# Optimization experiments

Measured on AMD Instinct MI355X. Metric: run time of the kernel, lower is better.

Reference implementation:

```python
import jax, jax.numpy as jnp
import numpy as np

# module hyperparams (match init_kwargs)
C_IN = 256
HEADS = 8
HEAD_DIM = 32
PW, PH = 4, 4
TOPK = 2
SIM_POW = 2.0
SIDE = 64
T = SIDE * SIDE
B = 16


def setup_inputs() -> dict:
    key = jax.random.key(0)
    ks = jax.random.split(key, 7)
    hd = HEADS * HEAD_DIM
    s = 1.0 / np.sqrt(C_IN)
    return {
        "x": jax.random.normal(ks[0], (T, B, C_IN), dtype=jnp.float32),
        "f_w": jax.random.uniform(ks[1], (hd, C_IN), jnp.float32, -s, s),
        "f_b": jax.random.uniform(ks[2], (hd,), jnp.float32, -s, s),
        "v_w": jax.random.uniform(ks[3], (hd, C_IN), jnp.float32, -s, s),
        "v_b": jax.random.uniform(ks[4], (hd,), jnp.float32, -s, s),
        "proj_w": jax.random.uniform(ks[5], (C_IN, hd), jnp.float32, -1.0 / np.sqrt(hd), 1.0 / np.sqrt(hd)),
        "proj_b": jax.random.uniform(ks[6], (C_IN,), jnp.float32, -1.0 / np.sqrt(hd), 1.0 / np.sqrt(hd)),
        "sim_alpha": jnp.ones((1,), jnp.float32),
        "sim_beta": jnp.zeros((1,), jnp.float32),
    }


def _l2norm(z):
    # F.normalize with eps=1e-12
    n = jnp.linalg.norm(z, axis=-1, keepdims=True)
    return z / jnp.maximum(n, 1e-12)


def reference(x, f_w, f_b, v_w, v_b, proj_w, proj_b, sim_alpha, sim_beta):
    t, b, c = x.shape
    side = SIDE
    H, D = HEADS, HEAD_DIM
    M = PW * PH

    xt = jnp.transpose(x, (1, 0, 2))  # [B, T, C]
    q = xt @ f_w.T + f_b              # [B, T, H*D] (1x1 conv)
    v = xt @ v_w.T + v_b

    def split_heads(z):
        # [B,T,H*D] -> [B*H, side, side, D]
        z = z.reshape(b, side, side, H, D)
        return jnp.transpose(z, (0, 3, 1, 2, 4)).reshape(b * H, side, side, D)

    q2 = split_heads(q)
    v2 = split_heads(v)

    def pool(z):
        # adaptive avg pool (side,side)->(PW,PH), side divisible by PW/PH
        z = z.reshape(b * H, PW, side // PW, PH, side // PH, D)
        return z.mean(axis=(2, 4)).reshape(b * H, M, D)

    centers = pool(q2)        # [BH, M, D]
    value_centers = pool(v2)  # [BH, M, D]
    q_tok = q2.reshape(b * H, t, D)
    v_tok = v2.reshape(b * H, t, D)

    sim = jax.nn.sigmoid(
        sim_beta + sim_alpha * jnp.einsum("bmd,btd->bmt", _l2norm(centers), _l2norm(q_tok))
    )  # [BH, M, T]

    k = min(TOPK, M)
    _, idx = jax.lax.top_k(jnp.transpose(sim, (0, 2, 1)), k)  # idx [BH, T, k] over centers
    mask = jax.nn.one_hot(idx, M, dtype=sim.dtype).sum(axis=2)  # [BH, T, M]
    sim = sim * jnp.transpose(mask, (0, 2, 1))
    if SIM_POW != 1.0:
        sim = sim ** SIM_POW
    sim = sim / (sim.sum(axis=1, keepdims=True) + 1e-6)

    centers_out = (jnp.einsum("bmt,btd->bmd", sim, v_tok) + value_centers) / (
        sim.sum(axis=2, keepdims=True) + 1.0
    )  # [BH, M, D]
    out_tok = jnp.einsum("bmt,bmd->btd", sim, centers_out)  # [BH, T, D]

    out = jnp.transpose(out_tok.reshape(b, H, side, side, D), (0, 2, 3, 1, 4)).reshape(b, t, H * D)
    out = out @ proj_w.T + proj_b  # [B, T, C]
    return jnp.transpose(out, (1, 0, 2))  # [T, B, C]
```

## Files before the change

### kernel.cpp

```cpp
#include <hip/hip_runtime.h>
#include <math.h>

#define T_SZ 4096
#define B_SZ 16
#define CIN 256
#define N_H 8
#define D_H 32
#define M_C 16
#define TAU 5e-5f
#define RCAP (1<<19)

typedef unsigned char u8;
typedef unsigned int uint;
typedef unsigned short ushort;

using frag_ab = __attribute__((ext_vector_type(8))) short;
using frag_c  = __attribute__((ext_vector_type(4))) float;

#define O_FWT   0
#define O_VWT   262144
#define O_WFH   524288
#define O_WFL   655360
#define O_WVH   786432
#define O_WVL   917504
#define O_WPH   1048576
#define O_WPL   1179648
#define O_PX    1310720
#define O_C64   1835008
#define O_C32   2359296
#define O_VC    2621440
#define O_COUT  2883584
#define O_GPART 3145728
#define O_CNT   5308416
#define O_LIST  5308672
#define O_SELM  7405824
#define O_SELW  8454400
#define O_XS    12648704
#define O_XSL   46203136
#define O_V     79757568

__device__ __forceinline__ uint bfr(float f){
  uint u = __float_as_uint(f);
  return (u + 0x7FFFu + ((u >> 16) & 1u)) >> 16;
}
__device__ __forceinline__ float bff(uint h){ return __uint_as_float(h << 16); }

__global__ void k_transpose(const float* __restrict__ fw, const float* __restrict__ vw,
                            float* __restrict__ fwT, float* __restrict__ vwT){
  int id = blockIdx.x * 256 + threadIdx.x;
  int mat = id >> 16; int rem = id & 65535;
  int j = rem >> 8, c = rem & 255;
  const float* src = (mat == 0) ? fw : vw;
  float* dst = (mat == 0) ? fwT : vwT;
  dst[c * 256 + j] = src[j * 256 + c];
}

__global__ void k_wsplit(const float* __restrict__ fw, const float* __restrict__ vw,
                         const float* __restrict__ pw,
                         ushort* __restrict__ fh, ushort* __restrict__ fl,
                         ushort* __restrict__ vh, ushort* __restrict__ vl,
                         ushort* __restrict__ ph, ushort* __restrict__ pl){
  int id = blockIdx.x * 256 + threadIdx.x;
  int mat = id >> 16, rem = id & 65535;
  const float* s = (mat == 0) ? fw : ((mat == 1) ? vw : pw);
  ushort* dh = (mat == 0) ? fh : ((mat == 1) ? vh : ph);
  ushort* dl = (mat == 0) ? fl : ((mat == 1) ? vl : pl);
  int n = rem >> 8, k = rem & 255;
  size_t po = ((size_t)((n >> 7) * 8 + (k >> 5))) * 4096
            + (size_t)(((k >> 3) & 3) * 128 + (n & 127)) * 8 + (k & 7);
  float a = s[rem];
  uint h = bfr(a);
  dh[po] = (ushort)h;
  dl[po] = (ushort)bfr(a - bff(h));
}

__global__ __launch_bounds__(256, 8) void k_xsplit(
    const float* __restrict__ x, ushort* __restrict__ xh, ushort* __restrict__ xl){
  int b = blockIdx.x >> 5, mt = blockIdx.x & 31;
  int row = threadIdx.x & 127, cg0 = threadIdx.x >> 7;
  int t = mt * 128 + row;
  const float* xr = x + ((size_t)t * B_SZ + b) * CIN;
  size_t base = (size_t)(b * 32 + mt) * 8 * 4096;
#pragma unroll 4
  for (int i = 0; i < 16; i++){
    int c8 = i * 2 + cg0;
    float4 a0 = *(const float4*)(xr + c8 * 8);
    float4 a1 = *(const float4*)(xr + c8 * 8 + 4);
    uint h0 = bfr(a0.x), h1 = bfr(a0.y), h2 = bfr(a0.z), h3 = bfr(a0.w);
    uint h4 = bfr(a1.x), h5 = bfr(a1.y), h6 = bfr(a1.z), h7 = bfr(a1.w);
    uint l0 = bfr(a0.x - bff(h0)), l1 = bfr(a0.y - bff(h1));
    uint l2 = bfr(a0.z - bff(h2)), l3 = bfr(a0.w - bff(h3));
    uint l4 = bfr(a1.x - bff(h4)), l5 = bfr(a1.y - bff(h5));
    uint l6 = bfr(a1.z - bff(h6)), l7 = bfr(a1.w - bff(h7));
    size_t off = base + (size_t)(c8 >> 2) * 4096 + (size_t)((c8 & 3) * 128 + row) * 8;
    *(uint4*)(xh + off) = make_uint4(h0 | (h1 << 16), h2 | (h3 << 16), h4 | (h5 << 16), h6 | (h7 << 16));
    *(uint4*)(xl + off) = make_uint4(l0 | (l1 << 16), l2 | (l3 << 16), l4 | (l5 << 16), l6 | (l7 << 16));
  }
}

__global__ void k_pool(const float* __restrict__ x, double* __restrict__ px){
  int b = blockIdx.x >> 4, m = blockIdx.x & 15;
  int pr = m >> 2, pc = m & 3;
  int c = threadIdx.x;
  double s = 0.0;
  for (int i = 0; i < 16; i++){
    int t0 = (pr * 16 + i) * 64 + pc * 16;
    const float* xr = x + ((size_t)t0 * B_SZ + b) * CIN + c;
    for (int jj = 0; jj < 16; jj++)
      s += (double)xr[(size_t)jj * B_SZ * CIN];
  }
  px[(size_t)(b * 16 + m) * 256 + c] = s * (1.0 / 256.0);
}

__global__ void k_centers(const double* __restrict__ px, const float* __restrict__ fwT,
                          const float* __restrict__ vwT, const float* __restrict__ fb,
                          const float* __restrict__ vb, double* __restrict__ c64,
                          float* __restrict__ c32, float* __restrict__ vc){
  int b = blockIdx.x >> 4, m = blockIdx.x & 15;
  int j = threadIdx.x;
  const double* pxr = px + (size_t)(b * 16 + m) * 256;
  double cq = (double)fb[j], cv = (double)vb[j];
  for (int c = 0; c < 256; c++){
    double p = pxr[c];
    cq += p * (double)fwT[c * 256 + j];
    cv += p * (double)vwT[c * 256 + j];
  }
  __shared__ double sq[256];
  __shared__ double snm[8];
  sq[j] = cq * cq;
  __syncthreads();
  int h = j >> 5, d = j & 31;
  if ((j & 31) == 0){
    double ts = 0.0;
    for (int dd = 0; dd < 32; dd++) ts += sq[h * 32 + dd];
    snm[h] = fmax(sqrt(ts), 1e-12);
  }
  __syncthreads();
  double nm = snm[h];
  size_t o = ((size_t)(b * N_H + h) * M_C + m) * D_H + d;
  double ch = cq / nm;
  c64[o] = ch; c32[o] = (float)ch; vc[o] = (float)cv;
}

#define TSZU 4096

__device__ __forceinline__ void stage_async(
    const ushort* __restrict__ At_h, const ushort* __restrict__ At_l,
    const ushort* __restrict__ Bt_h, const ushort* __restrict__ Bt_l,
    int kk, ushort* SM, int tid){
  int w = tid >> 6, lane = tid & 63;
  const ushort* src = (w == 0) ? At_h : (w == 1) ? At_l : (w == 2) ? Bt_h : Bt_l;
  ushort* dst = SM + w * TSZU;
  const ushort* g0 = src + (size_t)kk * 4096 + lane * 8;
#pragma unroll
  for (int j = 0; j < 8; j++){
    __builtin_amdgcn_global_load_lds(
        (const __attribute__((address_space(1))) void*)(g0 + j * 512),
        (__attribute__((address_space(3))) void*)(dst + j * 512), 16, 0, 0);
  }
}

__device__ __forceinline__ void compute_step(
    const ushort* SM, int wm, int wn, int li, int quad, frag_c acc[4][4]){
  const ushort* Ah = SM;            const ushort* Al = SM + TSZU;
  const ushort* Bh = SM + 2*TSZU;   const ushort* Bl = SM + 3*TSZU;
  frag_ab ah[4], al[4], bh[4], bl[4];
#pragma unroll
  for (int m = 0; m < 4; m++){
    int off = (quad * 128 + wm * 64 + m * 16 + li) * 8;
    ah[m] = *(const frag_ab*)&Ah[off];
    al[m] = *(const frag_ab*)&Al[off];
  }
#pragma unroll
  for (int n = 0; n < 4; n++){
    int off = (quad * 128 + wn * 64 + n * 16 + li) * 8;
    bh[n] = *(const frag_ab*)&Bh[off];
    bl[n] = *(const frag_ab*)&Bl[off];
  }
#pragma unroll
  for (int m = 0; m < 4; m++)
#pragma unroll
    for (int n = 0; n < 4; n++){
      acc[m][n] = __builtin_amdgcn_mfma_f32_16x16x32_bf16(ah[m], bh[n], acc[m][n], 0, 0, 0);
      acc[m][n] = __builtin_amdgcn_mfma_f32_16x16x32_bf16(ah[m], bl[n], acc[m][n], 0, 0, 0);
      acc[m][n] = __builtin_amdgcn_mfma_f32_16x16x32_bf16(al[m], bh[n], acc[m][n], 0, 0, 0);
    }
}

__device__ __forceinline__ void gemm_core(
    const ushort* __restrict__ At_h, const ushort* __restrict__ At_l,
    const ushort* __restrict__ Bt_h, const ushort* __restrict__ Bt_l,
    ushort* SM, frag_c acc[4][4], int tid){
  int li = tid & 15, quad = (tid & 63) >> 4;
  int w = tid >> 6, wm = w >> 1, wn = w & 1;
#pragma unroll
  for (int m = 0; m < 4; m++)
#pragma unroll
    for (int n = 0; n < 4; n++)
      acc[m][n] = frag_c{0.f, 0.f, 0.f, 0.f};
  for (int kk = 0; kk < 8; kk++){
    __syncthreads();
    stage_async(At_h, At_l, Bt_h, Bt_l, kk, SM, tid);
    __syncthreads();
    compute_step(SM, wm, wn, li, quad, acc);
  }
}

__global__ __launch_bounds__(256, 4) void k_gemm_store(
    const ushort* __restrict__ Ahg, const ushort* __restrict__ Alg,
    const ushort* __restrict__ Bh, const ushort* __restrict__ Bl,
    const float* __restrict__ bias,
    float* __restrict__ Out, int oStride, int oBMul){
  int bx = blockIdx.x;
  int nt = bx & 1, mt = (bx >> 1) & 31, b = bx >> 6;
  __shared__ ushort SM[4 * TSZU];
  frag_c acc[4][4];
  int tid = threadIdx.x;
  size_t aOff = (size_t)(b * 32 + mt) * 8 * 4096;
  size_t bOff = (size_t)nt * 8 * 4096;
  gemm_core(Ahg + aOff, Alg + aOff, Bh + bOff, Bl + bOff, SM, acc, tid);

  int li = tid & 15, quad = (tid & 63) >> 4;
  int w = tid >> 6, wm = w >> 1, wn = w & 1;
  int colBase = nt * 128 + wn * 64 + li;
  float bn[4];
#pragma unroll
  for (int n = 0; n < 4; n++) bn[n] = bias[colBase + n * 16];
#pragma unroll
  for (int m = 0; m < 4; m++){
    int row0 = mt * 128 + wm * 64 + m * 16 + quad * 4;
#pragma unroll
    for (int n = 0; n < 4; n++){
      int col = colBase + n * 16;
#pragma unroll
      for (int r = 0; r < 4; r++)
        Out[(size_t)(row0 + r) * oStride + (size_t)b * oBMul + col] = acc[m][n][r] + bn[n];
    }
  }
}

__global__ __launch_bounds__(256, 3) void k_gemm_qsim(
    const ushort* __restrict__ Ahg, const ushort* __restrict__ Alg,
    const ushort* __restrict__ Bh, const ushort* __restrict__ Bl,
    const float* __restrict__ bias, const float* __restrict__ c32,
    const float* __restrict__ salpha, const float* __restrict__ sbeta,
    u8* __restrict__ selm, float2* __restrict__ selw,
    int* __restrict__ cnt, unsigned int* __restrict__ list){
  int bx = blockIdx.x;
  int nt = bx & 1, mt = (bx >> 1) & 31, b = bx >> 6;
  __shared__ ushort SM[16896];
  __shared__ float cs[4][520];
  frag_c acc[4][4];
  int tid = threadIdx.x;
  for (int i = tid; i < 2048; i += 256){
    int hh = i >> 9, rem = i & 511;
    cs[hh][rem] = c32[(size_t)b * 4096 + (nt * 4 + hh) * 512 + rem];
  }
  size_t aOff = (size_t)(b * 32 + mt) * 8 * 4096;
  size_t bOff = (size_t)nt * 8 * 4096;
  gemm_core(Ahg + aOff, Alg + aOff, Bh + bOff, Bl + bOff, SM, acc, tid);

  int li = tid & 15, quad = (tid & 63) >> 4;
  int w = tid >> 6, wm = w >> 1, wn = w & 1;
  int colBase = nt * 128 + wn * 64 + li;
  float bn[4];
#pragma unroll
  for (int n = 0; n < 4; n++) bn[n] = bias[colBase + n * 16];
  float alpha = salpha[0], beta = sbeta[0];
  float* qbuf = (float*)SM;
  for (int half = 0; half < 2; half++){
    __syncthreads();
    if (wm == half){
#pragma unroll
      for (int m = 0; m < 4; m++)
#pragma unroll
        for (int n = 0; n < 4; n++)
#pragma unroll
          for (int r = 0; r < 4; r++)
            qbuf[(m * 16 + quad * 4 + r) * 132 + wn * 64 + n * 16 + li] = acc[m][n][r] + bn[n];
    }
    __syncthreads();
    int tok = tid >> 2, hh = tid & 3;
    int t = mt * 128 + half * 64 + tok;
    int h = nt * 4 + hh;
    float q[32];
    float ss = 0.f;
#pragma unroll
    for (int d = 0; d < 32; d += 4){
      float4 qv = *(const float4*)&qbuf[tok * 132 + hh * 32 + d];
      q[d] = qv.x; q[d + 1] = qv.y; q[d + 2] = qv.z; q[d + 3] = qv.w;
      ss += qv.x * qv.x + qv.y * qv.y + qv.z * qv.z + qv.w * qv.w;
    }
    float inv = 1.f / fmaxf(sqrtf(ss), 1e-12f);
    float s1 = -1e30f, s2 = -1e30f, s3 = -1e30f; int i1 = 0, i2 = 0;
#pragma unroll
    for (int m = 0; m < 16; m++){
      float dot = 0.f;
#pragma unroll
      for (int d = 0; d < 32; d += 4){
        float4 cv = *(const float4*)&cs[hh][m * 32 + d];
        dot = fmaf(q[d], cv.x, fmaf(q[d + 1], cv.y, fmaf(q[d + 2], cv.z, fmaf(q[d + 3], cv.w, dot))));
      }
      float z = beta + alpha * (dot * inv);
      float s = 1.f / (1.f + expf(-z));
      if (s > s1){ s3 = s2; s2 = s1; i2 = i1; s1 = s; i1 = m; }
      else if (s > s2){ s3 = s2; s2 = s; i2 = m; }
      else if (s > s3){ s3 = s; }
    }
    if (s2 - s3 < TAU){
      int idx = atomicAdd(cnt, 1);
      if (idx < RCAP) list[idx] = (((unsigned)(b * N_H + h)) << 12) | (unsigned)t;
    }
    float r1 = s1 * s1, r2 = s2 * s2;
    float den = r1 + r2 + 1e-6f;
    size_t so = (size_t)(b * N_H + h) * T_SZ + t;
    selm[so * 2] = (u8)i1; selm[so * 2 + 1] = (u8)i2;
    selw[so] = make_float2(r1 / den, r2 / den);
  }
}

__global__ __launch_bounds__(256, 4) void k_rescue(
    const float* __restrict__ x, const float* __restrict__ fw, const float* __restrict__ fb,
    const double* __restrict__ c64, const float* __restrict__ salpha, const float* __restrict__ sbeta,
    const int* __restrict__ cnt, const unsigned int* __restrict__ list,
    u8* __restrict__ selm, float2* __restrict__ selw){
  int n = *cnt; if (n > RCAP) n = RCAP;
  int lane = threadIdx.x & 63;
  int wid = (blockIdx.x * 256 + threadIdx.x) >> 6;
  int nw = gridDim.x * 4;
  double alpha = (double)salpha[0], beta = (double)sbeta[0];
  for (int i = wid; i < n; i += nw){
    unsigned e = list[i];
    int t = e & 4095; int bh = e >> 12; int b = bh >> 3, h = bh & 7;
    int d = lane & 31, half = lane >> 5;
    const float* xh = x + ((size_t)t * B_SZ + b) * CIN + half * 128;
    const float* wr = fw + (size_t)(h * 32 + d) * CIN + half * 128;
    double a0 = 0, a1 = 0, a2 = 0, a3 = 0;
#pragma unroll 4
    for (int c = 0; c < 128; c += 4){
      float4 xv = *(const float4*)(xh + c);
      float4 wv = *(const float4*)(wr + c);
      a0 += (double)xv.x * (double)wv.x;
      a1 += (double)xv.y * (double)wv.y;
      a2 += (double)xv.z * (double)wv.z;
      a3 += (double)xv.w * (double)wv.w;
    }
    double qd = (a0 + a1) + (a2 + a3);
    qd += __shfl_down(qd, 32);
    if (lane < 32) qd += (double)fb[h * 32 + d];
    else qd = 0.0;
    double ss = qd * qd;
#pragma unroll
    for (int off = 32; off; off >>= 1) ss += __shfl_xor(ss, off);
    double inv = 1.0 / fmax(sqrt(ss), 1e-12);
    const double* cb = c64 + (size_t)bh * (M_C * D_H);
    int m = lane & 15;
    double dot = 0.0;
#pragma unroll
    for (int dd = 0; dd < 32; dd++){
      double qv = __shfl(qd, dd);
      dot += qv * cb[m * 32 + dd];
    }
    double z = beta + alpha * (dot * inv);
    double s = 1.0 / (1.0 + exp(-z));
    double s1 = -1e300, s2 = -1e300; int i1 = 0, i2 = 0;
#pragma unroll
    for (int mm = 0; mm < 16; mm++){
      double sv = __shfl(s, mm);
      if (sv > s1){ s2 = s1; i2 = i1; s1 = sv; i1 = mm; }
      else if (sv > s2){ s2 = sv; i2 = mm; }
    }
    if (lane == 0){
      double r1 = s1 * s1, r2 = s2 * s2, den = r1 + r2 + 1e-6;
      size_t so = (size_t)bh * T_SZ + t;
      selm[so * 2] = (u8)i1; selm[so * 2 + 1] = (u8)i2;
      selw[so] = make_float2((float)(r1 / den), (float)(r2 / den));
    }
  }
}

__global__ __launch_bounds__(256, 4) void k_scatter(
    const float* __restrict__ v, const u8* __restrict__ selm, const float2* __restrict__ selw,
    float* __restrict__ gpart){
  int bh = blockIdx.x >> 3, chunk = blockIdx.x & 7;
  int b = bh >> 3, h = bh & 7;
  int tid = threadIdx.x;
  int mA = tid >> 5, mB = mA + 8, d = tid & 31;
  __shared__ uchar2 sm[512];
  __shared__ float2 sw[512];
  for (int i = tid; i < 512; i += 256){
    size_t so = (size_t)bh * T_SZ + chunk * 512 + i;
    sm[i] = make_uchar2(selm[so * 2], selm[so * 2 + 1]);
    sw[i] = selw[so];
  }
  __syncthreads();
  const float* vb = v + ((size_t)b * T_SZ + chunk * 512) * CIN + h * 32 + d;
  float accA = 0.f, accB = 0.f, cntA = 0.f, cntB = 0.f;
#pragma unroll 8
  for (int i = 0; i < 512; i++){
    float vv = vb[(size_t)i * CIN];
    uchar2 mm = sm[i];
    float2 w = sw[i];
    float wA = (mm.x == mA) ? w.x : ((mm.y == mA) ? w.y : 0.f);
    float wB = (mm.x == mB) ? w.x : ((mm.y == mB) ? w.y : 0.f);
    accA = fmaf(wA, vv, accA); cntA += wA;
    accB = fmaf(wB, vv, accB); cntB += wB;
  }
  float* gp = gpart + (size_t)(bh * 8 + chunk) * 528;
  gp[mA * 33 + d] = accA;
  gp[mB * 33 + d] = accB;
  if (d == 0){ gp[mA * 33 + 32] = cntA; gp[mB * 33 + 32] = cntB; }
}

__global__ void k_cfinal(const float* __restrict__ gpart, const float* __restrict__ vc,
                         float* __restrict__ cout){
  int id = blockIdx.x * 256 + threadIdx.x;
  int bh = id >> 9, rem = id & 511, m = rem >> 5, d = rem & 31;
  float num = 0.f, den = 0.f;
#pragma unroll
  for (int c = 0; c < 8; c++){
    const float* gp = gpart + (size_t)(bh * 8 + c) * 528 + m * 33;
    num += gp[d];
    den += gp[32];
  }
  cout[id] = (num + vc[id]) / (den + 1.0f);
}

__global__ __launch_bounds__(256, 4) void k_mix(
    const float* __restrict__ cout, const u8* __restrict__ selm, const float2* __restrict__ selw,
    ushort* __restrict__ OTh, ushort* __restrict__ OTl){
  int b = blockIdx.x >> 7, tt = blockIdx.x & 127;
  __shared__ float cs[8][516];
  int tid = threadIdx.x;
  for (int kth = 0; kth < 16; kth++){
    int i = kth * 256 + tid;
    cs[i >> 9][i & 511] = cout[(size_t)b * 4096 + i];
  }
  __syncthreads();
  int r = tid & 31, h = tid >> 5;
  int t = tt * 32 + r;
  int mt = t >> 7, row = t & 127;
  size_t so = (size_t)(b * N_H + h) * T_SZ + t;
  int m1 = selm[so * 2], m2 = selm[so * 2 + 1];
  float2 w = selw[so];
  size_t base = ((size_t)(b * 32 + mt) * 8 + h) * 4096 + (size_t)row * 8;
#pragma unroll
  for (int d = 0; d < 32; d += 8){
    float4 c1a = *(const float4*)&cs[h][m1 * 32 + d];
    float4 c2a = *(const float4*)&cs[h][m2 * 32 + d];
    float4 c1b = *(const float4*)&cs[h][m1 * 32 + d + 4];
    float4 c2b = *(const float4*)&cs[h][m2 * 32 + d + 4];
    float o0 = w.x * c1a.x + w.y * c2a.x, o1 = w.x * c1a.y + w.y * c2a.y;
    float o2 = w.x * c1a.z + w.y * c2a.z, o3 = w.x * c1a.w + w.y * c2a.w;
    float o4 = w.x * c1b.x + w.y * c2b.x, o5 = w.x * c1b.y + w.y * c2b.y;
    float o6 = w.x * c1b.z + w.y * c2b.z, o7 = w.x * c1b.w + w.y * c2b.w;
    uint h0 = bfr(o0), h1 = bfr(o1), h2 = bfr(o2), h3 = bfr(o3);
    uint h4 = bfr(o4), h5 = bfr(o5), h6 = bfr(o6), h7 = bfr(o7);
    uint l0 = bfr(o0 - bff(h0)), l1 = bfr(o1 - bff(h1));
    uint l2 = bfr(o2 - bff(h2)), l3 = bfr(o3 - bff(h3));
    uint l4 = bfr(o4 - bff(h4)), l5 = bfr(o5 - bff(h5));
    uint l6 = bfr(o6 - bff(h6)), l7 = bfr(o7 - bff(h7));
    size_t off = base + (size_t)(d >> 3) * 1024;
    *(uint4*)(OTh + off) = make_uint4(h0 | (h1 << 16), h2 | (h3 << 16), h4 | (h5 << 16), h6 | (h7 << 16));
    *(uint4*)(OTl + off) = make_uint4(l0 | (l1 << 16), l2 | (l3 << 16), l4 | (l5 << 16), l6 | (l7 << 16));
  }
}

extern "C" void kernel_launch(void* const* d_in, const int* in_sizes, int n_in,
                              void* d_out, int out_size, void* d_ws, size_t ws_size,
                              hipStream_t stream) {
  const float* x   = (const float*)d_in[0];
  const float* f_w = (const float*)d_in[1];
  const float* f_b = (const float*)d_in[2];
  const float* v_w = (const float*)d_in[3];
  const float* v_b = (const float*)d_in[4];
  const float* p_w = (const float*)d_in[5];
  const float* p_b = (const float*)d_in[6];
  const float* s_a = (const float*)d_in[7];
  const float* s_b = (const float*)d_in[8];
  float* out = (float*)d_out;
  char* ws = (char*)d_ws;

  float*  fwT  = (float*)(ws + O_FWT);
  float*  vwT  = (float*)(ws + O_VWT);
  ushort* wfh  = (ushort*)(ws + O_WFH);
  ushort* wfl  = (ushort*)(ws + O_WFL);
  ushort* wvh  = (ushort*)(ws + O_WVH);
  ushort* wvl  = (ushort*)(ws + O_WVL);
  ushort* wph  = (ushort*)(ws + O_WPH);
  ushort* wpl  = (ushort*)(ws + O_WPL);
  double* px   = (double*)(ws + O_PX);
  double* c64  = (double*)(ws + O_C64);
  float*  c32  = (float*)(ws + O_C32);
  float*  vc   = (float*)(ws + O_VC);
  float*  cout = (float*)(ws + O_COUT);
  float*  gpart= (float*)(ws + O_GPART);
  int*    cnt  = (int*)(ws + O_CNT);
  unsigned int* list = (unsigned int*)(ws + O_LIST);
  u8*     selm = (u8*)(ws + O_SELM);
  float2* selw = (float2*)(ws + O_SELW);
  ushort* xh   = (ushort*)(ws + O_XS);
  ushort* xl   = (ushort*)(ws + O_XSL);
  ushort* OTh  = (ushort*)(ws + O_XS);
  ushort* OTl  = (ushort*)(ws + O_XSL);
  float*  v    = (float*)(ws + O_V);

  hipMemsetAsync(ws + O_CNT, 0, 256, stream);
  k_transpose<<<512, 256, 0, stream>>>(f_w, v_w, fwT, vwT);
  k_wsplit<<<768, 256, 0, stream>>>(f_w, v_w, p_w, wfh, wfl, wvh, wvl, wph, wpl);
  k_xsplit<<<512, 256, 0, stream>>>(x, xh, xl);
  k_pool<<<256, 256, 0, stream>>>(x, px);
  k_centers<<<256, 256, 0, stream>>>(px, fwT, vwT, f_b, v_b, c64, c32, vc);
  k_gemm_qsim<<<1024, 256, 0, stream>>>(xh, xl, wfh, wfl, f_b, c32, s_a, s_b,
                                        selm, selw, cnt, list);
  k_gemm_store<<<1024, 256, 0, stream>>>(xh, xl, wvh, wvl, v_b, v, 256, T_SZ * CIN);
  k_rescue<<<256, 256, 0, stream>>>(x, f_w, f_b, c64, s_a, s_b, cnt, list, selm, selw);
  k_scatter<<<1024, 256, 0, stream>>>(v, selm, selw, gpart);
  k_cfinal<<<256, 256, 0, stream>>>(gpart, vc, cout);
  k_mix<<<2048, 256, 0, stream>>>(cout, selm, selw, OTh, OTl);
  k_gemm_store<<<1024, 256, 0, stream>>>(OTh, OTl, wph, wpl, p_b, out, 4096, 256);
}
```

Before: 392.8 us.

## Fuse Q and V projection GEMMs into one launch, load B fragments from global

The separate Q-similarity GEMM and V GEMM kernels are merged into one 2048-block kernel over a concatenated Q/V weight layout. Blocks with nt<2 run the similarity/top-2 epilogue in 32-token chunks, and the rest store V. The GEMM core now stages only the A tiles in LDS and reads B weight fragments straight from global memory. This cuts LDS size and one launch, and lets the sim epilogue overlap V tiles, at the cost of uncached global B reads and a serialized epilogue that uses only half the threads.

```diff
diff --git a/kernel.cpp b/kernel.cpp
--- a/kernel.cpp
+++ b/kernel.cpp
@@ -19,10 +19,8 @@
 
 #define O_FWT   0
 #define O_VWT   262144
-#define O_WFH   524288
-#define O_WFL   655360
-#define O_WVH   786432
-#define O_WVL   917504
+#define O_WQVH  524288
+#define O_WQVL  786432
 #define O_WPH   1048576
 #define O_WPL   1179648
 #define O_PX    1310720
@@ -57,15 +55,14 @@
 
 __global__ void k_wsplit(const float* __restrict__ fw, const float* __restrict__ vw,
                          const float* __restrict__ pw,
-                         ushort* __restrict__ fh, ushort* __restrict__ fl,
-                         ushort* __restrict__ vh, ushort* __restrict__ vl,
+                         ushort* __restrict__ qvh, ushort* __restrict__ qvl,
                          ushort* __restrict__ ph, ushort* __restrict__ pl){
   int id = blockIdx.x * 256 + threadIdx.x;
   int mat = id >> 16, rem = id & 65535;
   const float* s = (mat == 0) ? fw : ((mat == 1) ? vw : pw);
-  ushort* dh = (mat == 0) ? fh : ((mat == 1) ? vh : ph);
-  ushort* dl = (mat == 0) ? fl : ((mat == 1) ? vl : pl);
-  int n = rem >> 8, k = rem & 255;
+  ushort* dh = (mat < 2) ? qvh : ph;
+  ushort* dl = (mat < 2) ? qvl : pl;
+  int n = (rem >> 8) + ((mat == 1) ? 256 : 0), k = rem & 255;
   size_t po = ((size_t)((n >> 7) * 8 + (k >> 5))) * 4096
             + (size_t)(((k >> 3) & 3) * 128 + (n & 127)) * 8 + (k & 7);
   float a = s[rem];
@@ -142,57 +139,52 @@
   c64[o] = ch; c32[o] = (float)ch; vc[o] = (float)cv;
 }
 
-#define TSZU 4096
-
-__device__ __forceinline__ void stage_async(
+__device__ __forceinline__ void stage_A(
     const ushort* __restrict__ At_h, const ushort* __restrict__ At_l,
-    const ushort* __restrict__ Bt_h, const ushort* __restrict__ Bt_l,
-    int kk, ushort* SM, int tid){
+    int kk, ushort* Ah, ushort* Al, int tid){
   int w = tid >> 6, lane = tid & 63;
-  const ushort* src = (w == 0) ? At_h : (w == 1) ? At_l : (w == 2) ? Bt_h : Bt_l;
-  ushort* dst = SM + w * TSZU;
-  const ushort* g0 = src + (size_t)kk * 4096 + lane * 8;
-#pragma unroll
-  for (int j = 0; j < 8; j++){
+  const ushort* src = (w & 1) ? At_l : At_h;
+  ushort* dst = (w & 1) ? Al : Ah;
+  int segbase = (w >> 1) * 4;
+#pragma unroll
+  for (int jj = 0; jj < 4; jj++){
+    int off = (segbase + jj) * 512 + lane * 8;
     __builtin_amdgcn_global_load_lds(
-        (const __attribute__((address_space(1))) void*)(g0 + j * 512),
-        (__attribute__((address_space(3))) void*)(dst + j * 512), 16, 0, 0);
+        (const __attribute__((address_space(1))) void*)(src + (size_t)kk * 4096 + off),
+        (__attribute__((address_space(3))) void*)(dst + off), 16, 0, 0);
   }
 }
 
 __device__ __forceinline__ void compute_step(
-    const ushort* SM, int wm, int wn, int li, int quad, frag_c acc[4][4]){
-  const ushort* Ah = SM;            const ushort* Al = SM + TSZU;
-  const ushort* Bh = SM + 2*TSZU;   const ushort* Bl = SM + 3*TSZU;
-  frag_ab ah[4], al[4], bh[4], bl[4];
+    const ushort* Ah, const ushort* Al,
+    const ushort* __restrict__ Bt_h, const ushort* __restrict__ Bt_l, int kk,
+    int wm, int wn, int li, int quad, frag_c acc[4][4]){
+  frag_ab bh[4], bl[4];
+#pragma unroll
+  for (int n = 0; n < 4; n++){
+    size_t off = (size_t)kk * 4096 + (size_t)(quad * 128 + wn * 64 + n * 16 + li) * 8;
+    bh[n] = *(const frag_ab*)(Bt_h + off);
+    bl[n] = *(const frag_ab*)(Bt_l + off);
+  }
 #pragma unroll
   for (int m = 0; m < 4; m++){
-    int off = (quad * 128 + wm * 64 + m * 16 + li) * 8;
-    ah[m] = *(const frag_ab*)&Ah[off];
-    al[m] = *(const frag_ab*)&Al[off];
-  }
-#pragma unroll
-  for (int n = 0; n < 4; n++){
-    int off = (quad * 128 + wn * 64 + n * 16 + li) * 8;
-    bh[n] = *(const frag_ab*)&Bh[off];
-    bl[n] = *(const frag_ab*)&Bl[off];
-  }
-#pragma unroll
-  for (int m = 0; m < 4; m++)
+    int aoff = (quad * 128 + wm * 64 + m * 16 + li) * 8;
+    frag_ab amh = *(const frag_ab*)&Ah[aoff];
+    frag_ab aml = *(const frag_ab*)&Al[aoff];
 #pragma unroll
     for (int n = 0; n < 4; n++){
-      acc[m][n] = __builtin_amdgcn_mfma_f32_16x16x32_bf16(ah[m], bh[n], acc[m][n], 0, 0, 0);
-      acc[m][n] = __builtin_amdgcn_mfma_f32_16x16x32_bf16(ah[m], bl[n], acc[m][n], 0, 0, 0);
-      acc[m][n] = __builtin_amdgcn_mfma_f32_16x16x32_bf16(al[m], bh[n], acc[m][n], 0, 0, 0);
-    }
+      acc[m][n] = __builtin_amdgcn_mfma_f32_16x16x32_bf16(amh, bh[n], acc[m][n], 0, 0, 0);
+      acc[m][n] = __builtin_amdgcn_mfma_f32_16x16x32_bf16(amh, bl[n], acc[m][n], 0, 0, 0);
+      acc[m][n] = __builtin_amdgcn_mfma_f32_16x16x32_bf16(aml, bh[n], acc[m][n], 0, 0, 0);
+    }
+  }
 }
 
 __device__ __forceinline__ void gemm_core(
     const ushort* __restrict__ At_h, const ushort* __restrict__ At_l,
     const ushort* __restrict__ Bt_h, const ushort* __restrict__ Bt_l,
-    ushort* SM, frag_c acc[4][4], int tid){
-  int li = tid & 15, quad = (tid & 63) >> 4;
-  int w = tid >> 6, wm = w >> 1, wn = w & 1;
+    ushort* Ah, ushort* Al, frag_c acc[4][4], int tid,
+    int wm, int wn, int li, int quad){
 #pragma unroll
   for (int m = 0; m < 4; m++)
 #pragma unroll
@@ -200,28 +192,137 @@
       acc[m][n] = frag_c{0.f, 0.f, 0.f, 0.f};
   for (int kk = 0; kk < 8; kk++){
     __syncthreads();
-    stage_async(At_h, At_l, Bt_h, Bt_l, kk, SM, tid);
+    stage_A(At_h, At_l, kk, Ah, Al, tid);
     __syncthreads();
-    compute_step(SM, wm, wn, li, quad, acc);
-  }
-}
-
-__global__ __launch_bounds__(256, 4) void k_gemm_store(
+    compute_step(Ah, Al, Bt_h, Bt_l, kk, wm, wn, li, quad, acc);
+  }
+}
+
+__global__ __launch_bounds__(256, 4) void k_gemm_qv(
     const ushort* __restrict__ Ahg, const ushort* __restrict__ Alg,
     const ushort* __restrict__ Bh, const ushort* __restrict__ Bl,
-    const float* __restrict__ bias,
-    float* __restrict__ Out, int oStride, int oBMul){
+    const float* __restrict__ fb, const float* __restrict__ vb,
+    const float* __restrict__ c32,
+    const float* __restrict__ salpha, const float* __restrict__ sbeta,
+    u8* __restrict__ selm, float2* __restrict__ selw,
+    int* __restrict__ cnt, unsigned int* __restrict__ list,
+    float* __restrict__ vout){
+  int bx = blockIdx.x;
+  int nt = bx & 3, mt = (bx >> 2) & 31, b = bx >> 7;
+  __shared__ char LDSB[25216];
+  ushort* Ah = (ushort*)LDSB;
+  ushort* Al = (ushort*)(LDSB + 8192);
+  float* qbuf = (float*)LDSB;
+  float* cs   = (float*)(LDSB + 16896);
+  int tid = threadIdx.x;
+  int li = tid & 15, quad = (tid & 63) >> 4;
+  int w = tid >> 6, wm = w >> 1, wn = w & 1;
+  if (nt < 2){
+    for (int i = tid; i < 2048; i += 256){
+      int hh = i >> 9, rem = i & 511;
+      cs[hh * 520 + rem] = c32[(size_t)b * 4096 + (nt * 4 + hh) * 512 + rem];
+    }
+  }
+  frag_c acc[4][4];
+  size_t aOff = (size_t)(b * 32 + mt) * 8 * 4096;
+  size_t bOff = (size_t)nt * 8 * 4096;
+  gemm_core(Ahg + aOff, Alg + aOff, Bh + bOff, Bl + bOff, Ah, Al, acc, tid, wm, wn, li, quad);
+
+  if (nt >= 2){
+    int colBase = (nt - 2) * 128 + wn * 64 + li;
+    float bn[4];
+#pragma unroll
+    for (int n = 0; n < 4; n++) bn[n] = vb[colBase + n * 16];
+#pragma unroll
+    for (int m = 0; m < 4; m++){
+      int row0 = mt * 128 + wm * 64 + m * 16 + quad * 4;
+#pragma unroll
+      for (int n = 0; n < 4; n++){
+        int col = colBase + n * 16;
+#pragma unroll
+        for (int r = 0; r < 4; r++)
+          vout[((size_t)b * T_SZ + row0 + r) * CIN + col] = acc[m][n][r] + bn[n];
+      }
+    }
+    return;
+  }
+  int colBase = nt * 128 + wn * 64 + li;
+  float bn[4];
+#pragma unroll
+  for (int n = 0; n < 4; n++) bn[n] = fb[colBase + n * 16];
+  float alpha = salpha[0], beta = sbeta[0];
+  for (int q4 = 0; q4 < 4; q4++){
+    __syncthreads();
+    if (wm == (q4 >> 1)){
+      int mb = (q4 & 1) * 2;
+#pragma unroll
+      for (int mm = 0; mm < 2; mm++){
+#pragma unroll
+        for (int n = 0; n < 4; n++)
+#pragma unroll
+          for (int r = 0; r < 4; r++)
+            qbuf[(mm * 16 + quad * 4 + r) * 132 + wn * 64 + n * 16 + li] = acc[mb + mm][n][r] + bn[n];
+      }
+    }
+    __syncthreads();
+    if (tid < 128){
+      int tok = tid >> 2, hh = tid & 3;
+      int t = mt * 128 + q4 * 32 + tok;
+      int h = nt * 4 + hh;
+      float q[32];
+      float ss = 0.f;
+#pragma unroll
+      for (int d = 0; d < 32; d += 4){
+        float4 qv = *(const float4*)&qbuf[tok * 132 + hh * 32 + d];
+        q[d] = qv.x; q[d + 1] = qv.y; q[d + 2] = qv.z; q[d + 3] = qv.w;
+        ss += qv.x * qv.x + qv.y * qv.y + qv.z * qv.z + qv.w * qv.w;
+      }
+      float inv = 1.f / fmaxf(sqrtf(ss), 1e-12f);
+      float s1 = -1e30f, s2 = -1e30f, s3 = -1e30f; int i1 = 0, i2 = 0;
+#pragma unroll
+      for (int m = 0; m < 16; m++){
+        float dot = 0.f;
+#pragma unroll
+        for (int d = 0; d < 32; d += 4){
+          float4 cv = *(const float4*)&cs[hh * 520 + m * 32 + d];
+          dot = fmaf(q[d], cv.x, fmaf(q[d + 1], cv.y, fmaf(q[d + 2], cv.z, fmaf(q[d + 3], cv.w, dot))));
+        }
+        float z = beta + alpha * (dot * inv);
+        float s = 1.f / (1.f + expf(-z));
+        if (s > s1){ s3 = s2; s2 = s1; i2 = i1; s1 = s; i1 = m; }
+        else if (s > s2){ s3 = s2; s2 = s; i2 = m; }
+        else if (s > s3){ s3 = s; }
+      }
+      if (s2 - s3 < TAU){
+        int idx = atomicAdd(cnt, 1);
+        if (idx < RCAP) list[idx] = (((unsigned)(b * N_H + h)) << 12) | (unsigned)t;
+      }
+      float r1 = s1 * s1, r2 = s2 * s2;
+      float den = r1 + r2 + 1e-6f;
+      size_t so = (size_t)(b * N_H + h) * T_SZ + t;
+      selm[so * 2] = (u8)i1; selm[so * 2 + 1] = (u8)i2;
+      selw[so] = make_float2(r1 / den, r2 / den);
+    }
+  }
+}
+
+__global__ __launch_bounds__(256, 4) void k_gemm_proj(
+    const ushort* __restrict__ Ahg, const ushort* __restrict__ Alg,
+    const ushort* __restrict__ Bh, const ushort* __restrict__ Bl,
+    const float* __restrict__ bias, float* __restrict__ Out){
   int bx = blockIdx.x;
   int nt = bx & 1, mt = (bx >> 1) & 31, b = bx >> 6;
-  __shared__ ushort SM[4 * TSZU];
+  __shared__ ushort SM[8192];
+  ushort* Ah = SM;
+  ushort* Al = SM + 4096;
+  int tid = threadIdx.x;
+  int li = tid & 15, quad = (tid & 63) >> 4;
+  int w = tid >> 6, wm = w >> 1, wn = w & 1;
   frag_c acc[4][4];
-  int tid = threadIdx.x;
   size_t aOff = (size_t)(b * 32 + mt) * 8 * 4096;
   size_t bOff = (size_t)nt * 8 * 4096;
-  gemm_core(Ahg + aOff, Alg + aOff, Bh + bOff, Bl + bOff, SM, acc, tid);
-
-  int li = tid & 15, quad = (tid & 63) >> 4;
-  int w = tid >> 6, wm = w >> 1, wn = w & 1;
+  gemm_core(Ahg + aOff, Alg + aOff, Bh + bOff, Bl + bOff, Ah, Al, acc, tid, wm, wn, li, quad);
+
   int colBase = nt * 128 + wn * 64 + li;
   float bn[4];
 #pragma unroll
@@ -234,88 +335,8 @@
       int col = colBase + n * 16;
 #pragma unroll
       for (int r = 0; r < 4; r++)
-        Out[(size_t)(row0 + r) * oStride + (size_t)b * oBMul + col] = acc[m][n][r] + bn[n];
-    }
-  }
-}
-
-__global__ __launch_bounds__(256, 3) void k_gemm_qsim(
-    const ushort* __restrict__ Ahg, const ushort* __restrict__ Alg,
-    const ushort* __restrict__ Bh, const ushort* __restrict__ Bl,
-    const float* __restrict__ bias, const float* __restrict__ c32,
-    const float* __restrict__ salpha, const float* __restrict__ sbeta,
-    u8* __restrict__ selm, float2* __restrict__ selw,
-    int* __restrict__ cnt, unsigned int* __restrict__ list){
-  int bx = blockIdx.x;
-  int nt = bx & 1, mt = (bx >> 1) & 31, b = bx >> 6;
-  __shared__ ushort SM[16896];
-  __shared__ float cs[4][520];
-  frag_c acc[4][4];
-  int tid = threadIdx.x;
-  for (int i = tid; i < 2048; i += 256){
-    int hh = i >> 9, rem = i & 511;
-    cs[hh][rem] = c32[(size_t)b * 4096 + (nt * 4 + hh) * 512 + rem];
-  }
-  size_t aOff = (size_t)(b * 32 + mt) * 8 * 4096;
-  size_t bOff = (size_t)nt * 8 * 4096;
-  gemm_core(Ahg + aOff, Alg + aOff, Bh + bOff, Bl + bOff, SM, acc, tid);
-
-  int li = tid & 15, quad = (tid & 63) >> 4;
-  int w = tid >> 6, wm = w >> 1, wn = w & 1;
-  int colBase = nt * 128 + wn * 64 + li;
-  float bn[4];
-#pragma unroll
-  for (int n = 0; n < 4; n++) bn[n] = bias[colBase + n * 16];
-  float alpha = salpha[0], beta = sbeta[0];
-  float* qbuf = (float*)SM;
-  for (int half = 0; half < 2; half++){
-    __syncthreads();
-    if (wm == half){
-#pragma unroll
-      for (int m = 0; m < 4; m++)
-#pragma unroll
-        for (int n = 0; n < 4; n++)
-#pragma unroll
-          for (int r = 0; r < 4; r++)
-            qbuf[(m * 16 + quad * 4 + r) * 132 + wn * 64 + n * 16 + li] = acc[m][n][r] + bn[n];
-    }
-    __syncthreads();
-    int tok = tid >> 2, hh = tid & 3;
-    int t = mt * 128 + half * 64 + tok;
-    int h = nt * 4 + hh;
-    float q[32];
-    float ss = 0.f;
-#pragma unroll
-    for (int d = 0; d < 32; d += 4){
-      float4 qv = *(const float4*)&qbuf[tok * 132 + hh * 32 + d];
-      q[d] = qv.x; q[d + 1] = qv.y; q[d + 2] = qv.z; q[d + 3] = qv.w;
-      ss += qv.x * qv.x + qv.y * qv.y + qv.z * qv.z + qv.w * qv.w;
-    }
-    float inv = 1.f / fmaxf(sqrtf(ss), 1e-12f);
-    float s1 = -1e30f, s2 = -1e30f, s3 = -1e30f; int i1 = 0, i2 = 0;
-#pragma unroll
-    for (int m = 0; m < 16; m++){
-      float dot = 0.f;
-#pragma unroll
-      for (int d = 0; d < 32; d += 4){
-        float4 cv = *(const float4*)&cs[hh][m * 32 + d];
-        dot = fmaf(q[d], cv.x, fmaf(q[d + 1], cv.y, fmaf(q[d + 2], cv.z, fmaf(q[d + 3], cv.w, dot))));
-      }
-      float z = beta + alpha * (dot * inv);
-      float s = 1.f / (1.f + expf(-z));
-      if (s > s1){ s3 = s2; s2 = s1; i2 = i1; s1 = s; i1 = m; }
-      else if (s > s2){ s3 = s2; s2 = s; i2 = m; }
-      else if (s > s3){ s3 = s; }
-    }
-    if (s2 - s3 < TAU){
-      int idx = atomicAdd(cnt, 1);
-      if (idx < RCAP) list[idx] = (((unsigned)(b * N_H + h)) << 12) | (unsigned)t;
-    }
-    float r1 = s1 * s1, r2 = s2 * s2;
-    float den = r1 + r2 + 1e-6f;
-    size_t so = (size_t)(b * N_H + h) * T_SZ + t;
-    selm[so * 2] = (u8)i1; selm[so * 2 + 1] = (u8)i2;
-    selw[so] = make_float2(r1 / den, r2 / den);
+        Out[(size_t)(row0 + r) * 4096 + (size_t)b * 256 + col] = acc[m][n][r] + bn[n];
+    }
   }
 }
 
@@ -483,10 +504,8 @@
 
   float*  fwT  = (float*)(ws + O_FWT);
   float*  vwT  = (float*)(ws + O_VWT);
-  ushort* wfh  = (ushort*)(ws + O_WFH);
-  ushort* wfl  = (ushort*)(ws + O_WFL);
-  ushort* wvh  = (ushort*)(ws + O_WVH);
-  ushort* wvl  = (ushort*)(ws + O_WVL);
+  ushort* wqvh = (ushort*)(ws + O_WQVH);
+  ushort* wqvl = (ushort*)(ws + O_WQVL);
   ushort* wph  = (ushort*)(ws + O_WPH);
   ushort* wpl  = (ushort*)(ws + O_WPL);
   double* px   = (double*)(ws + O_PX);
@@ -507,16 +526,15 @@
 
   hipMemsetAsync(ws + O_CNT, 0, 256, stream);
   k_transpose<<<512, 256, 0, stream>>>(f_w, v_w, fwT, vwT);
-  k_wsplit<<<768, 256, 0, stream>>>(f_w, v_w, p_w, wfh, wfl, wvh, wvl, wph, wpl);
+  k_wsplit<<<768, 256, 0, stream>>>(f_w, v_w, p_w, wqvh, wqvl, wph, wpl);
   k_xsplit<<<512, 256, 0, stream>>>(x, xh, xl);
   k_pool<<<256, 256, 0, stream>>>(x, px);
   k_centers<<<256, 256, 0, stream>>>(px, fwT, vwT, f_b, v_b, c64, c32, vc);
-  k_gemm_qsim<<<1024, 256, 0, stream>>>(xh, xl, wfh, wfl, f_b, c32, s_a, s_b,
-                                        selm, selw, cnt, list);
-  k_gemm_store<<<1024, 256, 0, stream>>>(xh, xl, wvh, wvl, v_b, v, 256, T_SZ * CIN);
+  k_gemm_qv<<<2048, 256, 0, stream>>>(xh, xl, wqvh, wqvl, f_b, v_b, c32, s_a, s_b,
+                                      selm, selw, cnt, list, v);
   k_rescue<<<256, 256, 0, stream>>>(x, f_w, f_b, c64, s_a, s_b, cnt, list, selm, selw);
   k_scatter<<<1024, 256, 0, stream>>>(v, selm, selw, gpart);
   k_cfinal<<<256, 256, 0, stream>>>(gpart, vc, cout);
   k_mix<<<2048, 256, 0, stream>>>(cout, selm, selw, OTh, OTl);
-  k_gemm_store<<<1024, 256, 0, stream>>>(OTh, OTl, wph, wpl, p_b, out, 4096, 256);
-}
+  k_gemm_proj<<<1024, 256, 0, stream>>>(OTh, OTl, wph, wpl, p_b, out);
+}
```

Measured after the change: 569.7 us. +45.0%, slower.
